# Optimization experiments

Measured on AMD Instinct MI355X. Metric: run time of the kernel, lower is better.

## Reference

```python
import jax, jax.numpy as jnp
import numpy as np

KH, KW = 3, 3
KK = KH * KW
PAD = 1
STRIDE = 1


def setup_inputs() -> dict:
    key = jax.random.key(0)
    k1, k2, k3 = jax.random.split(key, 3)
    x = jax.random.normal(k1, (4, 64, 224, 224), jnp.float32)
    weight = jax.random.normal(k2, (64, 64, KH, KW), jnp.float32) * 0.05
    bias = jax.random.normal(k3, (64,), jnp.float32)
    return {"x": x, "weight": weight, "bias": bias}


def reference(x, weight, bias):
    B, C, H, W = x.shape
    # --- conv output (the wrapper delegates this to the wrapped conv) ---
    y = jax.lax.conv_general_dilated(
        x, weight,
        window_strides=(STRIDE, STRIDE),
        padding=((PAD, PAD), (PAD, PAD)),
        dimension_numbers=("NCHW", "OIHW", "NCHW"),
    ) + bias[None, :, None, None]

    # --- zero-count histogram (groups=1; torch code's [:, :, :, 0, 0] indexing
    # selects group 0 / out-channel 0, so only weight[0] matters) ---
    # patches: (B, C*KK, Ho, Wo), channel-major ordering (channel, then kh, kw)
    patches = jax.lax.conv_general_dilated_patches(
        x, (KH, KW), (STRIDE, STRIDE), ((PAD, PAD), (PAD, PAD)))
    Ho, Wo = patches.shape[2], patches.shape[3]
    patches = patches.reshape(B, C, KK, Ho, Wo)
    prod = patches * weight[0].reshape(1, C, KK, 1, 1)  # patch * weight, oc=0
    # num_of_zeros = kk - count_nonzero over the kernel window
    zeros = KK - jnp.count_nonzero(prod, axis=2)  # (B, C, Ho, Wo), int
    # accumulate one_hot(zeros).sum over (batch, h, w) per input channel
    zf = zeros.transpose(1, 0, 2, 3).reshape(C, -1)  # (C, B*Ho*Wo)
    hist = jnp.zeros((C, KK + 1), jnp.float32).at[
        jnp.arange(C)[:, None], zf].add(1.0)
    return y, hist
```

## Files before the change

kernel.cpp:

```cpp
#include <hip/hip_runtime.h>

#define HW 224
#define HW2 50176
#define NCH 64
#define NPIX (4 * HW2)
#define CONV_OUT_ELEMS (4 * NCH * HW2)
#define ZCAP 8192

typedef short bf16x8 __attribute__((ext_vector_type(8)));
typedef float f32x4 __attribute__((ext_vector_type(4)));

__device__ __forceinline__ unsigned short f2bf(float f) {
    unsigned u = __float_as_uint(f);
    u += 0x7FFFu + ((u >> 16) & 1u);
    return (unsigned short)(u >> 16);
}


__global__ __launch_bounds__(256) void prep_fused(
    const float* __restrict__ xf, const float* __restrict__ w,
    unsigned short* __restrict__ xbf, unsigned short* __restrict__ wbufA,
    int* __restrict__ zcnt, unsigned int* __restrict__ zlist)
{
    const int tid = threadIdx.x;
    const int bid = blockIdx.x;

    if (bid >= 6272) {
        const int o = (bid - 6272) * 256 + tid;
        if (o < 18 * 2048) {
            const int j    = o & 7;
            const int lane = (o >> 3) & 63;
            const int n    = lane & 15;
            const int q    = lane >> 4;
            const int mg   = (o >> 9) & 3;
            const int k    = o >> 11;
            const int tap  = k >> 1;
            const int half = k & 1;
            const int ci   = half * 32 + q * 8 + j;
            const int co   = mg * 16 + n;
            wbufA[o] = f2bf(w[(co * 64 + ci) * 9 + tap]);
        }
        return;
    }

    const int pix = bid * 32 + (tid >> 3);
    const int oct = tid & 7;
    const int b   = pix / HW2;
    const int rem = pix - b * HW2;
    const float* src = xf + (size_t)(b * NCH + oct * 8) * HW2 + rem;

    float fv[8];
#pragma unroll
    for (int j = 0; j < 8; ++j) fv[j] = src[(size_t)j * HW2];

    bf16x8 v;
#pragma unroll
    for (int j = 0; j < 8; ++j) v[j] = (short)f2bf(fv[j]);
    *reinterpret_cast<bf16x8*>(xbf + (size_t)pix * 64 + oct * 8) = v;

    bool anyz = false;
#pragma unroll
    for (int j = 0; j < 8; ++j) anyz |= (fv[j] == 0.0f);
    if (__builtin_expect(anyz, 0)) {
        const int yy = rem / HW;
        const int xx = rem - yy * HW;
#pragma unroll
        for (int j = 0; j < 8; ++j) {
            if (fv[j] == 0.0f) {
                const int idx = atomicAdd(zcnt, 1);
                if (idx < ZCAP) {
                    const int ci = oct * 8 + j;
                    zlist[idx] = ((unsigned)b << 22) | ((unsigned)ci << 16)
                               | ((unsigned)yy << 8) | (unsigned)xx;
                }
            }
        }
    }
}

__global__ __launch_bounds__(256, 3) void conv_mfma_v2(
    const unsigned short* __restrict__ xbf,
    const unsigned short* __restrict__ wbufA,
    const float* __restrict__ bias, float* __restrict__ y)
{
    __shared__ alignas(16) unsigned short xs[340 * 64];

    const int tid  = threadIdx.x;
    const int wv   = tid >> 6;
    const int lane = tid & 63;
    const int n    = lane & 15;
    const int q    = lane >> 4;
    const int c0   = blockIdx.x * 32;
    const int r0   = blockIdx.y * 8;
    const int b    = blockIdx.z;

    for (int i = tid; i < 2720; i += 256) {
        const int pos = i >> 3;
        const int blk = i & 7;
        const int rr  = pos / 34;
        const int cc  = pos - rr * 34;
        const int gy  = r0 + rr - 1;
        const int gx  = c0 + cc - 1;
        const int phys = pos * 8 + (blk ^ (pos & 7));
        bf16x8 v = (bf16x8){0, 0, 0, 0, 0, 0, 0, 0};
        if ((unsigned)gy < (unsigned)HW && (unsigned)gx < (unsigned)HW)
            v = *reinterpret_cast<const bf16x8*>(
                xbf + ((size_t)(b * HW + gy) * HW + gx) * 64 + blk * 8);
        *reinterpret_cast<bf16x8*>(xs + phys * 8) = v;
    }
    __syncthreads();

    f32x4 acc[4][4];
#pragma unroll
    for (int mg = 0; mg < 4; ++mg)
#pragma unroll
        for (int g = 0; g < 4; ++g) acc[mg][g] = (f32x4){0.f, 0.f, 0.f, 0.f};

#pragma unroll
    for (int tap = 0; tap < 9; ++tap) {
        const int dh = tap / 3, dw = tap % 3;
#pragma unroll
        for (int half = 0; half < 2; ++half) {
            const int k = tap * 2 + half;
            bf16x8 a[4];
#pragma unroll
            for (int mg = 0; mg < 4; ++mg)
                a[mg] = *reinterpret_cast<const bf16x8*>(
                    wbufA + (k * 4 + mg) * 512 + lane * 8);
#pragma unroll
            for (int g = 0; g < 4; ++g) {
                const int pos = (2 * wv + (g >> 1) + dh) * 34
                              + (g & 1) * 16 + dw + n;
                const int phys = pos * 8 + ((half * 4 + q) ^ (pos & 7));
                const bf16x8 bf =
                    *reinterpret_cast<const bf16x8*>(xs + phys * 8);
#pragma unroll
                for (int mg = 0; mg < 4; ++mg)
                    acc[mg][g] = __builtin_amdgcn_mfma_f32_16x16x32_bf16(
                        a[mg], bf, acc[mg][g], 0, 0, 0);
            }
        }
    }

#pragma unroll
    for (int g = 0; g < 4; ++g) {
        const int row = r0 + 2 * wv + (g >> 1);
        const int col = c0 + (g & 1) * 16 + n;
#pragma unroll
        for (int mg = 0; mg < 4; ++mg) {
#pragma unroll
            for (int rg = 0; rg < 4; ++rg) {
                const int co = mg * 16 + q * 4 + rg;
                y[((size_t)(b * NCH + co) * HW + row) * HW + col] =
                    acc[mg][g][rg] + bias[co];
            }
        }
    }
}

__global__ __launch_bounds__(256) void hist_final(
    const float* __restrict__ x, const float* __restrict__ w,
    const int* __restrict__ zcnt, const unsigned int* __restrict__ zlist,
    float* __restrict__ hist)
{
    __shared__ int lh[640];
    const int tid = threadIdx.x;
    for (int i = tid; i < 640; i += 256) lh[i] = 0;
    __syncthreads();

    if (tid < 64) {
        const int c = tid;
        float wk[9];
#pragma unroll
        for (int k = 0; k < 9; ++k) wk[k] = w[c * 9 + k];
        int bins[10];
#pragma unroll
        for (int k = 0; k < 10; ++k) bins[k] = 0;
#pragma unroll
        for (int rcat = 0; rcat < 3; ++rcat) {
#pragma unroll
            for (int scat = 0; scat < 3; ++scat) {
                int z = 0;
#pragma unroll
                for (int k = 0; k < 9; ++k) {
                    const int kh = k / 3, kw = k % 3;
                    const bool oob =
                        (rcat == 0 && kh == 0) || (rcat == 2 && kh == 2) ||
                        (scat == 0 && kw == 0) || (scat == 2 && kw == 2);
                    z += (oob || wk[k] == 0.0f) ? 1 : 0;
                }
                const int cnt =
                    4 * (rcat == 1 ? 222 : 1) * (scat == 1 ? 222 : 1);
                bins[z] += cnt;
            }
        }
#pragma unroll
        for (int k = 0; k < 10; ++k) lh[c * 10 + k] = bins[k];
    }
    __syncthreads();

    const int L = min(*zcnt, ZCAP);
    for (int p = tid; p < L * 9; p += 256) {
        const int e = p / 9, t = p - e * 9;
        const unsigned ent = zlist[e];
        const int b  = (int)(ent >> 22);
        const int c  = (int)(ent >> 16) & 63;
        const int zy = (int)(ent >> 8) & 255;
        const int zx = (int)ent & 255;
        const int kh = t / 3, kw = t % 3;
        const int r = zy - kh + 1, s = zx - kw + 1;
        if ((unsigned)r >= (unsigned)HW || (unsigned)s >= (unsigned)HW)
            continue;
        bool first = true;
        for (int e2 = 0; e2 < e && first; ++e2) {
            const unsigned ent2 = zlist[e2];
            if ((ent2 >> 16) == (ent >> 16)) {
                const int y2 = (int)(ent2 >> 8) & 255;
                const int x2 = (int)ent2 & 255;
                if ((unsigned)(y2 - r + 1) < 3u && (unsigned)(x2 - s + 1) < 3u)
                    first = false;
            }
        }
        if (!first) continue;

        const float* plane = x + (size_t)(b * NCH + c) * HW2;
        int zb = 0, zt = 0;
#pragma unroll
        for (int k = 0; k < 9; ++k) {
            const int kh2 = k / 3, kw2 = k % 3;
            const int yy = r + kh2 - 1, xx = s + kw2 - 1;
            const bool oob = (unsigned)yy >= (unsigned)HW ||
                             (unsigned)xx >= (unsigned)HW;
            const bool w0 = (w[c * 9 + k] == 0.0f);
            const bool x0 = !oob && (plane[yy * HW + xx] == 0.0f);
            zb += (oob || w0) ? 1 : 0;
            zt += (oob || w0 || x0) ? 1 : 0;
        }
        if (zb != zt) {
            atomicAdd(&lh[c * 10 + zb], -1);
            atomicAdd(&lh[c * 10 + zt], 1);
        }
    }
    __syncthreads();
    for (int i = tid; i < 640; i += 256) hist[i] = (float)lh[i];
}

__global__ void prep_weights_fb(const float* __restrict__ w,
                                unsigned short* __restrict__ wbuf) {
    const int o = blockIdx.x * 256 + threadIdx.x;
    if (o >= 2 * 9 * 4 * 16 * 32) return;
    const int ci = o & 31;
    const int t1 = o >> 5;
    const int co = t1 & 15;
    const int t2 = t1 >> 4;
    const int mg = t2 & 3;
    const int t3 = t2 >> 2;
    const int tap = t3 % 9;
    const int chunk = t3 / 9;
    wbuf[o] = f2bf(w[((mg * 16 + co) * 64 + (chunk * 32 + ci)) * 9 + tap]);
}

__global__ __launch_bounds__(256, 2) void conv_mfma_fb(
    const float* __restrict__ x, const unsigned short* __restrict__ wbuf,
    const float* __restrict__ bias, float* __restrict__ y)
{
    __shared__ alignas(16) unsigned short xs[340 * 32];
    const int tid  = threadIdx.x;
    const int wv   = tid >> 6;
    const int lane = tid & 63;
    const int n    = lane & 15;
    const int q    = lane >> 4;
    const int c0   = blockIdx.x * 32;
    const int r0   = blockIdx.y * 8;
    const int b    = blockIdx.z;

    f32x4 acc[4][4];
#pragma unroll
    for (int mg = 0; mg < 4; ++mg)
#pragma unroll
        for (int g = 0; g < 4; ++g) acc[mg][g] = (f32x4){0.f, 0.f, 0.f, 0.f};

    for (int chunk = 0; chunk < 2; ++chunk) {
        if (chunk) __syncthreads();
        const int ci0 = chunk * 32;
        for (int i = tid; i < 1360; i += 256) {
            const int ci8 = i / 340;
            const int pos = i - ci8 * 340;
            const int r   = pos / 34;
            const int c   = pos - r * 34;
            const int gy  = r0 + r - 1;
            const int gx  = c0 + c - 1;
            bf16x8 v;
            if ((unsigned)gy < (unsigned)HW && (unsigned)gx < (unsigned)HW) {
                const float* src =
                    x + ((size_t)(b * NCH + ci0 + ci8 * 8) * HW + gy) * HW + gx;
#pragma unroll
                for (int j = 0; j < 8; ++j) v[j] = (short)f2bf(src[(size_t)j * HW2]);
            } else {
#pragma unroll
                for (int j = 0; j < 8; ++j) v[j] = 0;
            }
            *reinterpret_cast<bf16x8*>(&xs[pos * 32 + ci8 * 8]) = v;
        }
        __syncthreads();

#pragma unroll
        for (int tap = 0; tap < 9; ++tap) {
            const int dh = tap / 3, dw = tap % 3;
            bf16x8 a[4];
#pragma unroll
            for (int mg = 0; mg < 4; ++mg) {
                const unsigned short* ap =
                    wbuf + ((chunk * 9 + tap) * 4 + mg) * 512 + n * 32 + q * 8;
                a[mg] = *reinterpret_cast<const bf16x8*>(ap);
            }
#pragma unroll
            for (int g = 0; g < 4; ++g) {
                const int rl = 2 * wv + (g >> 1) + dh;
                const int cl = (g & 1) * 16 + dw + n;
                const bf16x8 bf =
                    *reinterpret_cast<const bf16x8*>(&xs[(rl * 34 + cl) * 32 + q * 8]);
#pragma unroll
                for (int mg = 0; mg < 4; ++mg)
                    acc[mg][g] = __builtin_amdgcn_mfma_f32_16x16x32_bf16(
                        a[mg], bf, acc[mg][g], 0, 0, 0);
            }
        }
    }

#pragma unroll
    for (int g = 0; g < 4; ++g) {
        const int row = r0 + 2 * wv + (g >> 1);
        const int col = c0 + (g & 1) * 16 + n;
#pragma unroll
        for (int mg = 0; mg < 4; ++mg) {
#pragma unroll
            for (int rg = 0; rg < 4; ++rg) {
                const int co = mg * 16 + q * 4 + rg;
                y[((size_t)(b * NCH + co) * HW + row) * HW + col] =
                    acc[mg][g][rg] + bias[co];
            }
        }
    }
}

__global__ __launch_bounds__(256) void hist_v2(
    const float* __restrict__ x, const float* __restrict__ w,
    float* __restrict__ hist)
{
    __shared__ int lh[10];
    const int tid = threadIdx.x;
    const int col = tid;
    const int rg  = blockIdx.x;
    const int c   = blockIdx.y;
    const int b   = blockIdx.z;
    if (tid < 10) lh[tid] = 0;
    __syncthreads();

    int h[10];
#pragma unroll
    for (int k = 0; k < 10; ++k) h[k] = 0;

    if (col < HW) {
        const float* plane = x + (size_t)(b * NCH + c) * HW2;
        float wk[9];
#pragma unroll
        for (int k = 0; k < 9; ++k) wk[k] = w[c * 9 + k];

        const bool vl = col > 0, vr = col < HW - 1;
        const int r0 = rg * 28;
        float u0, u1, u2, m0, m1, m2;
        if (r0 > 0) {
            const float* p = plane + (size_t)(r0 - 1) * HW + col;
            u0 = vl ? p[-1] : 0.f; u1 = p[0]; u2 = vr ? p[1] : 0.f;
        } else { u0 = u1 = u2 = 0.f; }
        {
            const float* p = plane + (size_t)r0 * HW + col;
            m0 = vl ? p[-1] : 0.f; m1 = p[0]; m2 = vr ? p[1] : 0.f;
        }

        for (int r = r0; r < r0 + 28; ++r) {
            float d0, d1, d2;
            if (r + 1 < HW) {
                const float* p = plane + (size_t)(r + 1) * HW + col;
                d0 = vl ? p[-1] : 0.f; d1 = p[0]; d2 = vr ? p[1] : 0.f;
            } else { d0 = d1 = d2 = 0.f; }

            int cnt = 0;
            cnt += (u0 * wk[0] != 0.f); cnt += (u1 * wk[1] != 0.f); cnt += (u2 * wk[2] != 0.f);
            cnt += (m0 * wk[3] != 0.f); cnt += (m1 * wk[4] != 0.f); cnt += (m2 * wk[5] != 0.f);
            cnt += (d0 * wk[6] != 0.f); cnt += (d1 * wk[7] != 0.f); cnt += (d2 * wk[8] != 0.f);
            const int z = 9 - cnt;
#pragma unroll
            for (int k = 0; k < 10; ++k) h[k] += (z == k);
            u0 = m0; u1 = m1; u2 = m2; m0 = d0; m1 = d1; m2 = d2;
        }
    }

#pragma unroll
    for (int k = 0; k < 10; ++k) {
        int v = h[k];
        v += __shfl_xor(v, 32); v += __shfl_xor(v, 16); v += __shfl_xor(v, 8);
        v += __shfl_xor(v, 4);  v += __shfl_xor(v, 2);  v += __shfl_xor(v, 1);
        if ((tid & 63) == 0 && v != 0) atomicAdd(&lh[k], v);
    }
    __syncthreads();
    if (tid < 10 && lh[tid] > 0)
        atomicAdd(&hist[c * 10 + tid], (float)lh[tid]);
}

extern "C" void kernel_launch(void* const* d_in, const int* in_sizes, int n_in,
                              void* d_out, int out_size, void* d_ws, size_t ws_size,
                              hipStream_t stream) {
    const float* x    = (const float*)d_in[0];
    const float* w    = (const float*)d_in[1];
    const float* bias = (const float*)d_in[2];
    float* y    = (float*)d_out;
    float* hist = (float*)d_out + CONV_OUT_ELEMS;

    const size_t XBF_OFF = 73728;
    const size_t ZC_OFF  = XBF_OFF + (size_t)NPIX * 64 * 2;
    const size_t ZL_OFF  = ZC_OFF + 64;
    const size_t NEED    = ZL_OFF + (size_t)ZCAP * 4;

    if (ws_size >= NEED) {
        unsigned short* wbufA = (unsigned short*)d_ws;
        unsigned short* xbf   = (unsigned short*)((char*)d_ws + XBF_OFF);
        int* zcnt             = (int*)((char*)d_ws + ZC_OFF);
        unsigned int* zlist   = (unsigned int*)((char*)d_ws + ZL_OFF);

        hipMemsetAsync(zcnt, 0, sizeof(int), stream);
        prep_fused<<<6416, 256, 0, stream>>>(x, w, xbf, wbufA, zcnt, zlist);
        conv_mfma_v2<<<dim3(7, 28, 4), 256, 0, stream>>>(xbf, wbufA, bias, y);
        hist_final<<<1, 256, 0, stream>>>(x, w, zcnt, zlist, hist);
    } else {
        hipMemsetAsync(hist, 0, 64 * 10 * sizeof(float), stream);
        unsigned short* wbuf = (unsigned short*)d_ws;
        prep_weights_fb<<<144, 256, 0, stream>>>(w, wbuf);
        conv_mfma_fb<<<dim3(7, 28, 4), 256, 0, stream>>>(x, wbuf, bias, y);
        hist_v2<<<dim3(8, 64, 4), 256, 0, stream>>>(x, w, hist);
    }
}
```

Before: 142.9 us.

## Fuse fp32-to-bf16 input conversion and zero scan into conv tile load

Removes the separate prep pass that wrote a bf16 NHWC copy of the input. The conv kernel now reads fp32 NCHW directly while staging its halo tile, converts to bf16 in registers, and records zero positions, restricted to interior tile pixels so none is counted twice. The zero counter is reset inside the weight prep kernel instead of by a memset. This saves a full write and read of the intermediate tensor and one launch, but the tile loads become strided fp32 gathers, and halo pixels are read about 1.3x over across tiles.

```diff
diff --git a/kernel.cpp b/kernel.cpp
--- a/kernel.cpp
+++ b/kernel.cpp
@@ -17,71 +17,30 @@
 }
 
 
-__global__ __launch_bounds__(256) void prep_fused(
-    const float* __restrict__ xf, const float* __restrict__ w,
-    unsigned short* __restrict__ xbf, unsigned short* __restrict__ wbufA,
+__global__ __launch_bounds__(256) void prep_weights_v2(
+    const float* __restrict__ w, unsigned short* __restrict__ wbufA,
+    int* __restrict__ zcnt) {
+    const int o = blockIdx.x * 256 + threadIdx.x;
+    if (o == 0) *zcnt = 0;
+    if (o >= 18 * 2048) return;
+    const int j    = o & 7;
+    const int lane = (o >> 3) & 63;
+    const int n    = lane & 15;
+    const int q    = lane >> 4;
+    const int mg   = (o >> 9) & 3;
+    const int k    = o >> 11;
+    const int tap  = k >> 1;
+    const int half = k & 1;
+    const int ci   = half * 32 + q * 8 + j;
+    const int co   = mg * 16 + n;
+    wbufA[o] = f2bf(w[(co * 64 + ci) * 9 + tap]);
+}
+
+__global__ __launch_bounds__(256, 3) void conv_fused(
+    const float* __restrict__ xf,
+    const unsigned short* __restrict__ wbufA,
+    const float* __restrict__ bias, float* __restrict__ y,
     int* __restrict__ zcnt, unsigned int* __restrict__ zlist)
-{
-    const int tid = threadIdx.x;
-    const int bid = blockIdx.x;
-
-    if (bid >= 6272) {
-        const int o = (bid - 6272) * 256 + tid;
-        if (o < 18 * 2048) {
-            const int j    = o & 7;
-            const int lane = (o >> 3) & 63;
-            const int n    = lane & 15;
-            const int q    = lane >> 4;
-            const int mg   = (o >> 9) & 3;
-            const int k    = o >> 11;
-            const int tap  = k >> 1;
-            const int half = k & 1;
-            const int ci   = half * 32 + q * 8 + j;
-            const int co   = mg * 16 + n;
-            wbufA[o] = f2bf(w[(co * 64 + ci) * 9 + tap]);
-        }
-        return;
-    }
-
-    const int pix = bid * 32 + (tid >> 3);
-    const int oct = tid & 7;
-    const int b   = pix / HW2;
-    const int rem = pix - b * HW2;
-    const float* src = xf + (size_t)(b * NCH + oct * 8) * HW2 + rem;
-
-    float fv[8];
-#pragma unroll
-    for (int j = 0; j < 8; ++j) fv[j] = src[(size_t)j * HW2];
-
-    bf16x8 v;
-#pragma unroll
-    for (int j = 0; j < 8; ++j) v[j] = (short)f2bf(fv[j]);
-    *reinterpret_cast<bf16x8*>(xbf + (size_t)pix * 64 + oct * 8) = v;
-
-    bool anyz = false;
-#pragma unroll
-    for (int j = 0; j < 8; ++j) anyz |= (fv[j] == 0.0f);
-    if (__builtin_expect(anyz, 0)) {
-        const int yy = rem / HW;
-        const int xx = rem - yy * HW;
-#pragma unroll
-        for (int j = 0; j < 8; ++j) {
-            if (fv[j] == 0.0f) {
-                const int idx = atomicAdd(zcnt, 1);
-                if (idx < ZCAP) {
-                    const int ci = oct * 8 + j;
-                    zlist[idx] = ((unsigned)b << 22) | ((unsigned)ci << 16)
-                               | ((unsigned)yy << 8) | (unsigned)xx;
-                }
-            }
-        }
-    }
-}
-
-__global__ __launch_bounds__(256, 3) void conv_mfma_v2(
-    const unsigned short* __restrict__ xbf,
-    const unsigned short* __restrict__ wbufA,
-    const float* __restrict__ bias, float* __restrict__ y)
 {
     __shared__ alignas(16) unsigned short xs[340 * 64];
 
@@ -95,17 +54,41 @@
     const int b    = blockIdx.z;
 
     for (int i = tid; i < 2720; i += 256) {
-        const int pos = i >> 3;
-        const int blk = i & 7;
+        const int oct = i / 340;
+        const int pos = i - oct * 340;
         const int rr  = pos / 34;
         const int cc  = pos - rr * 34;
         const int gy  = r0 + rr - 1;
         const int gx  = c0 + cc - 1;
-        const int phys = pos * 8 + (blk ^ (pos & 7));
+        const int phys = pos * 8 + (oct ^ (pos & 7));
         bf16x8 v = (bf16x8){0, 0, 0, 0, 0, 0, 0, 0};
-        if ((unsigned)gy < (unsigned)HW && (unsigned)gx < (unsigned)HW)
-            v = *reinterpret_cast<const bf16x8*>(
-                xbf + ((size_t)(b * HW + gy) * HW + gx) * 64 + blk * 8);
+        if ((unsigned)gy < (unsigned)HW && (unsigned)gx < (unsigned)HW) {
+            const float* src =
+                xf + ((size_t)(b * NCH + oct * 8) * HW + gy) * HW + gx;
+            float fv[8];
+#pragma unroll
+            for (int j = 0; j < 8; ++j) fv[j] = src[(size_t)j * HW2];
+#pragma unroll
+            for (int j = 0; j < 8; ++j) v[j] = (short)f2bf(fv[j]);
+            bool anyz = false;
+#pragma unroll
+            for (int j = 0; j < 8; ++j) anyz |= (fv[j] == 0.0f);
+            if (__builtin_expect(anyz, 0) &&
+                rr >= 1 && rr <= 8 && cc >= 1 && cc <= 32) {
+#pragma unroll
+                for (int j = 0; j < 8; ++j) {
+                    if (fv[j] == 0.0f) {
+                        const int idx = atomicAdd(zcnt, 1);
+                        if (idx < ZCAP) {
+                            const int ci = oct * 8 + j;
+                            zlist[idx] = ((unsigned)b << 22)
+                                       | ((unsigned)ci << 16)
+                                       | ((unsigned)gy << 8) | (unsigned)gx;
+                        }
+                    }
+                }
+            }
+        }
         *reinterpret_cast<bf16x8*>(xs + phys * 8) = v;
     }
     __syncthreads();
@@ -418,20 +401,18 @@
     float* y    = (float*)d_out;
     float* hist = (float*)d_out + CONV_OUT_ELEMS;
 
-    const size_t XBF_OFF = 73728;
-    const size_t ZC_OFF  = XBF_OFF + (size_t)NPIX * 64 * 2;
-    const size_t ZL_OFF  = ZC_OFF + 64;
-    const size_t NEED    = ZL_OFF + (size_t)ZCAP * 4;
+    const size_t ZC_OFF = 73728;
+    const size_t ZL_OFF = ZC_OFF + 64;
+    const size_t NEED   = ZL_OFF + (size_t)ZCAP * 4;
 
     if (ws_size >= NEED) {
         unsigned short* wbufA = (unsigned short*)d_ws;
-        unsigned short* xbf   = (unsigned short*)((char*)d_ws + XBF_OFF);
         int* zcnt             = (int*)((char*)d_ws + ZC_OFF);
         unsigned int* zlist   = (unsigned int*)((char*)d_ws + ZL_OFF);
 
-        hipMemsetAsync(zcnt, 0, sizeof(int), stream);
-        prep_fused<<<6416, 256, 0, stream>>>(x, w, xbf, wbufA, zcnt, zlist);
-        conv_mfma_v2<<<dim3(7, 28, 4), 256, 0, stream>>>(xbf, wbufA, bias, y);
+        prep_weights_v2<<<144, 256, 0, stream>>>(w, wbufA, zcnt);
+        conv_fused<<<dim3(7, 28, 4), 256, 0, stream>>>(
+            x, wbufA, bias, y, zcnt, zlist);
         hist_final<<<1, 256, 0, stream>>>(x, w, zcnt, zlist, hist);
     } else {
         hipMemsetAsync(hist, 0, 64 * 10 * sizeof(float), stream);
```

After: 140.0 us. -2.0%, faster.

## Use direct global-to-LDS loads and 7-row tiles in conv kernel

Applied to the files above, without the earlier changes.

The conv kernel now stages the input halo tile into shared memory with global_load_lds, which skips the register round trip. The source block index is pre-swizzled so the LDS layout stays the same as before. The tile height drops from 8 to 7 rows so the LDS footprint shrinks, the grid grows to 32 row-blocks, and the occupancy hint goes from 3 to 4 blocks. In exchange, the last wave computes a duplicated row that is thrown away (about 1/8 wasted MFMA work), and out-of-bounds halo slots are zero-filled with normal LDS stores mixed in with the async loads.

```diff
diff --git a/kernel.cpp b/kernel.cpp
--- a/kernel.cpp
+++ b/kernel.cpp
@@ -7,6 +7,13 @@
 #define CONV_OUT_ELEMS (4 * NCH * HW2)
 #define ZCAP 8192
 
+#define TH 7
+#define TW 32
+#define LHH 9
+#define LWW 34
+#define NPOS 306
+#define NGRAN (NPOS * 8)
+
 typedef short bf16x8 __attribute__((ext_vector_type(8)));
 typedef float f32x4 __attribute__((ext_vector_type(4)));
 
@@ -14,6 +21,14 @@
     unsigned u = __float_as_uint(f);
     u += 0x7FFFu + ((u >> 16) & 1u);
     return (unsigned short)(u >> 16);
+}
+
+__device__ __forceinline__ void gload16(const unsigned short* src,
+                                        unsigned short* dst_uniform) {
+    __builtin_amdgcn_global_load_lds(
+        (const __attribute__((address_space(1))) unsigned int*)src,
+        (__attribute__((address_space(3))) unsigned int*)dst_uniform,
+        16, 0, 0);
 }
 
 
@@ -78,35 +93,43 @@
     }
 }
 
-__global__ __launch_bounds__(256, 3) void conv_mfma_v2(
+__global__ __launch_bounds__(256, 4) void conv_fused(
     const unsigned short* __restrict__ xbf,
     const unsigned short* __restrict__ wbufA,
     const float* __restrict__ bias, float* __restrict__ y)
 {
-    __shared__ alignas(16) unsigned short xs[340 * 64];
+    __shared__ alignas(16) unsigned short xs[NPOS * 64];
 
     const int tid  = threadIdx.x;
     const int wv   = tid >> 6;
     const int lane = tid & 63;
     const int n    = lane & 15;
     const int q    = lane >> 4;
-    const int c0   = blockIdx.x * 32;
-    const int r0   = blockIdx.y * 8;
+    const int c0   = blockIdx.x * TW;
+    const int r0   = blockIdx.y * TH;
     const int b    = blockIdx.z;
 
-    for (int i = tid; i < 2720; i += 256) {
-        const int pos = i >> 3;
-        const int blk = i & 7;
-        const int rr  = pos / 34;
-        const int cc  = pos - rr * 34;
-        const int gy  = r0 + rr - 1;
-        const int gx  = c0 + cc - 1;
-        const int phys = pos * 8 + (blk ^ (pos & 7));
-        bf16x8 v = (bf16x8){0, 0, 0, 0, 0, 0, 0, 0};
-        if ((unsigned)gy < (unsigned)HW && (unsigned)gx < (unsigned)HW)
-            v = *reinterpret_cast<const bf16x8*>(
-                xbf + ((size_t)(b * HW + gy) * HW + gx) * 64 + blk * 8);
-        *reinterpret_cast<bf16x8*>(xs + phys * 8) = v;
+#pragma unroll
+    for (int it = 0; it < 10; ++it) {
+        const int s = it * 256 + tid;
+        if (it < 9 || s < NGRAN) {
+            const int pos = s >> 3;
+            const int bq  = s & 7;
+            const int rr  = pos / LWW;
+            const int cc  = pos - rr * LWW;
+            const int gy  = r0 + rr - 1;
+            const int gx  = c0 + cc - 1;
+            const int blk = bq ^ (pos & 7);
+            unsigned short* dstb = xs + (size_t)(it * 256 + wv * 64) * 8;
+            if ((unsigned)gy < (unsigned)HW && (unsigned)gx < (unsigned)HW) {
+                const unsigned short* src =
+                    xbf + ((size_t)(b * HW + gy) * HW + gx) * 64 + blk * 8;
+                gload16(src, dstb);
+            } else {
+                *reinterpret_cast<bf16x8*>(xs + (size_t)s * 8) =
+                    (bf16x8){0, 0, 0, 0, 0, 0, 0, 0};
+            }
+        }
     }
     __syncthreads();
 
@@ -115,6 +138,9 @@
     for (int mg = 0; mg < 4; ++mg)
 #pragma unroll
         for (int g = 0; g < 4; ++g) acc[mg][g] = (f32x4){0.f, 0.f, 0.f, 0.f};
+
+    const int rw0 = 2 * wv;
+    const int rw1 = (2 * wv + 1 > TH - 1) ? TH - 1 : 2 * wv + 1;
 
 #pragma unroll
     for (int tap = 0; tap < 9; ++tap) {
@@ -129,8 +155,8 @@
                     wbufA + (k * 4 + mg) * 512 + lane * 8);
 #pragma unroll
             for (int g = 0; g < 4; ++g) {
-                const int pos = (2 * wv + (g >> 1) + dh) * 34
-                              + (g & 1) * 16 + dw + n;
+                const int rI  = (g >> 1) ? rw1 : rw0;
+                const int pos = (rI + dh) * LWW + (g & 1) * 16 + dw + n;
                 const int phys = pos * 8 + ((half * 4 + q) ^ (pos & 7));
                 const bf16x8 bf =
                     *reinterpret_cast<const bf16x8*>(xs + phys * 8);
@@ -144,15 +170,18 @@
 
 #pragma unroll
     for (int g = 0; g < 4; ++g) {
-        const int row = r0 + 2 * wv + (g >> 1);
-        const int col = c0 + (g & 1) * 16 + n;
-#pragma unroll
-        for (int mg = 0; mg < 4; ++mg) {
-#pragma unroll
-            for (int rg = 0; rg < 4; ++rg) {
-                const int co = mg * 16 + q * 4 + rg;
-                y[((size_t)(b * NCH + co) * HW + row) * HW + col] =
-                    acc[mg][g][rg] + bias[co];
+        const int rt = 2 * wv + (g >> 1);
+        if (rt < TH) {
+            const int row = r0 + rt;
+            const int col = c0 + (g & 1) * 16 + n;
+#pragma unroll
+            for (int mg = 0; mg < 4; ++mg) {
+#pragma unroll
+                for (int rg = 0; rg < 4; ++rg) {
+                    const int co = mg * 16 + q * 4 + rg;
+                    y[((size_t)(b * NCH + co) * HW + row) * HW + col] =
+                        acc[mg][g][rg] + bias[co];
+                }
             }
         }
     }
@@ -431,7 +460,7 @@
 
         hipMemsetAsync(zcnt, 0, sizeof(int), stream);
         prep_fused<<<6416, 256, 0, stream>>>(x, w, xbf, wbufA, zcnt, zlist);
-        conv_mfma_v2<<<dim3(7, 28, 4), 256, 0, stream>>>(xbf, wbufA, bias, y);
+        conv_fused<<<dim3(7, 32, 4), 256, 0, stream>>>(xbf, wbufA, bias, y);
         hist_final<<<1, 256, 0, stream>>>(x, w, zcnt, zlist, hist);
     } else {
         hipMemsetAsync(hist, 0, 64 * 10 * sizeof(float), stream);
```

New measurement: 132.9 us. -7.0%, faster.
